# Kernel optimization log

Measured on AMD Instinct MI355X. Metric: run time of the kernel, lower is better.

The kernel has to match this reference:

```python
import jax, jax.numpy as jnp
import numpy as np

B, L, D = 256, 1000, 512
V = 670091 + 1          # output_size + 1 dummy/padding row
PAD = V - 1             # padding_idx = output_size


def setup_inputs() -> dict:
    key = jax.random.key(0)
    k1, k2, k3, k4 = jax.random.split(key, 4)
    embed = jax.random.normal(k1, (B, D), dtype=jnp.float32)
    shortlist = jax.random.randint(k2, (B, L), 0, V, dtype=jnp.int64)
    # learned params (kaiming-ish scale); padding row zeroed as in reset_parameters
    weight = (jax.random.normal(k3, (V, D), dtype=jnp.float32) * 0.02).at[PAD].set(0.0)
    bias = (jax.random.normal(k4, (V, 1), dtype=jnp.float32) * 0.02).at[PAD].set(0.0)
    return {"embed": embed, "shortlist": shortlist, "weight": weight, "bias": bias}


def reference(embed, shortlist, weight, bias):
    # F.embedding gather: [B, L, D]
    short_weights = weight[shortlist]
    # matmul(embed.unsqueeze(1), short_weights.permute(0,2,1)).squeeze() -> [B, L]
    out = jnp.einsum('bd,bld->bl', embed, short_weights)
    # short_bias gather [B, L, 1] -> permuted/added -> [B, L]
    out = out + bias[shortlist, 0]
    return out
```

## Files before the change

### kernel.cpp

```cpp
#include <hip/hip_runtime.h>
#include <hip/hip_bf16.h>


#define BB 256
#define LL 1000
#define DD 512
#define LPB 40
#define ITERS 10

__global__ __launch_bounds__(256) void sparse_linear_kernel(
    const float* __restrict__ embed,
    const int*   __restrict__ shortlist,
    const float* __restrict__ weight,
    const float* __restrict__ bias,
    float*       __restrict__ out)
{
    const int b    = blockIdx.y;
    const int lane = threadIdx.x & 63;
    const int wave = threadIdx.x >> 6;

    const float4* e4 = reinterpret_cast<const float4*>(embed + (size_t)b * DD + lane * 8);
    const float4 e0 = e4[0];
    const float4 e1 = e4[1];

    const int lbase = blockIdx.x * LPB + wave;

    int pidx = 0;
    if (lane < ITERS)
        pidx = shortlist[(size_t)b * LL + lbase + 4 * lane];

    #pragma unroll
    for (int i = 0; i < ITERS; i += 2) {
        const int idx0 = __shfl(pidx, i);
        const int idx1 = __shfl(pidx, i + 1);

        float bval = 0.0f;
        if (lane == 0) bval = bias[idx0];
        if (lane == 1) bval = bias[idx1];

        const float4* wa = reinterpret_cast<const float4*>(weight + (size_t)idx0 * DD + lane * 8);
        const float4* wb = reinterpret_cast<const float4*>(weight + (size_t)idx1 * DD + lane * 8);
        const float4 a0 = wa[0];
        const float4 a1 = wa[1];
        const float4 c0 = wb[0];
        const float4 c1 = wb[1];

        float s0 = e0.x * a0.x + e0.y * a0.y + e0.z * a0.z + e0.w * a0.w
                 + e1.x * a1.x + e1.y * a1.y + e1.z * a1.z + e1.w * a1.w;
        float s1 = e0.x * c0.x + e0.y * c0.y + e0.z * c0.z + e0.w * c0.w
                 + e1.x * c1.x + e1.y * c1.y + e1.z * c1.z + e1.w * c1.w;

        #pragma unroll
        for (int off = 32; off > 0; off >>= 1) {
            s0 += __shfl_down(s0, off);
            s1 += __shfl_down(s1, off);
        }

        const float b1v = __shfl(bval, 1);
        if (lane == 0) {
            out[(size_t)b * LL + lbase + 4 * i]       = s0 + bval;
            out[(size_t)b * LL + lbase + 4 * (i + 1)] = s1 + b1v;
        }
    }
}

extern "C" void kernel_launch(void* const* d_in, const int* in_sizes, int n_in,
                              void* d_out, int out_size, void* d_ws, size_t ws_size,
                              hipStream_t stream) {
    const float* embed     = (const float*)d_in[0];
    const int*   shortlist = (const int*)  d_in[1];
    const float* weight    = (const float*)d_in[2];
    const float* bias      = (const float*)d_in[3];
    float*       out       = (float*)d_out;

    dim3 grid((LL + LPB - 1) / LPB, BB);
    sparse_linear_kernel<<<grid, 256, 0, stream>>>(embed, shortlist, weight, bias, out);
}
```

Baseline: 86.11 us.

## Split gather into vocabulary-range passes to improve cache locality of weight rows

Launches the kernel three times, each pass processing only shortlist indices within one third of the vocabulary, using a ballot mask to select matching rows per wave. The aim is to shrink the weight working set per pass (about 457MB total split into roughly 150MB chunks) so that duplicate row fetches hit in the large last-level cache. In exchange it adds three launches, rereads the shortlist and embed three times, and leaves waves partially idle through divergent while loops.

```diff
diff --git a/kernel.cpp b/kernel.cpp
--- a/kernel.cpp
+++ b/kernel.cpp
@@ -5,15 +5,18 @@
 #define BB 256
 #define LL 1000
 #define DD 512
+#define VV 670092
 #define LPB 40
 #define ITERS 10
+#define NPASS 3
 
-__global__ __launch_bounds__(256) void sparse_linear_kernel(
+__global__ __launch_bounds__(256) void sparse_linear_pass(
     const float* __restrict__ embed,
     const int*   __restrict__ shortlist,
     const float* __restrict__ weight,
     const float* __restrict__ bias,
-    float*       __restrict__ out)
+    float*       __restrict__ out,
+    int lo, int hi)
 {
     const int b    = blockIdx.y;
     const int lane = threadIdx.x & 63;
@@ -26,13 +29,27 @@
     const int lbase = blockIdx.x * LPB + wave;
 
     int pidx = 0;
-    if (lane < ITERS)
+    bool in_range = false;
+    if (lane < ITERS) {
         pidx = shortlist[(size_t)b * LL + lbase + 4 * lane];
+        in_range = (pidx >= lo) && (pidx < hi);
+    }
 
-    #pragma unroll
-    for (int i = 0; i < ITERS; i += 2) {
-        const int idx0 = __shfl(pidx, i);
-        const int idx1 = __shfl(pidx, i + 1);
+    unsigned long long mask = __ballot(in_range);
+
+    float* orow = out + (size_t)b * LL + lbase;
+
+    while (mask) {
+        const int p0 = __ffsll(mask) - 1;
+        mask &= mask - 1;
+        int p1 = -1;
+        if (mask) {
+            p1 = __ffsll(mask) - 1;
+            mask &= mask - 1;
+        }
+
+        const int idx0 = __shfl(pidx, p0);
+        const int idx1 = __shfl(pidx, p1 >= 0 ? p1 : p0);
 
         float bval = 0.0f;
         if (lane == 0) bval = bias[idx0];
@@ -58,8 +75,9 @@
 
         const float b1v = __shfl(bval, 1);
         if (lane == 0) {
-            out[(size_t)b * LL + lbase + 4 * i]       = s0 + bval;
-            out[(size_t)b * LL + lbase + 4 * (i + 1)] = s1 + b1v;
+            orow[4 * p0] = s0 + bval;
+            if (p1 >= 0)
+                orow[4 * p1] = s1 + b1v;
         }
     }
 }
@@ -74,5 +92,9 @@
     float*       out       = (float*)d_out;
 
     dim3 grid((LL + LPB - 1) / LPB, BB);
-    sparse_linear_kernel<<<grid, 256, 0, stream>>>(embed, shortlist, weight, bias, out);
+    const int bounds[NPASS + 1] = {0, VV / 3, 2 * (VV / 3), VV};
+    for (int p = 0; p < NPASS; ++p) {
+        sparse_linear_pass<<<grid, 256, 0, stream>>>(
+            embed, shortlist, weight, bias, out, bounds[p], bounds[p + 1]);
+    }
 }
```

Result: slower. 97.59 us (+13.3%).
